# Kernel optimization log

Hardware: AMD Instinct MI355X
Metric: run time of the kernel (lower is better)

Reference implementation:

```python
import jax, jax.numpy as jnp
import numpy as np

G = 144          # fine grid size per axis
N = 200000       # active fine voxels
C_IN = 96
C_UP = C_IN // 3 # 32
C_OUT = 64
EPS = 1e-5


def _build_maps():
    rng = np.random.default_rng(0)
    lin = rng.choice(G ** 3, size=N, replace=False)
    coords = np.stack(np.unravel_index(lin, (G, G, G)), axis=1).astype(np.int64)  # [N,3]
    # coarse coords = unique parents (stride-2 downsample), inverse gives parent index per fine voxel
    coarse, up_src = np.unique(coords // 2, axis=0, return_inverse=True)
    up_off = ((coords[:, 0] % 2) * 2 + coords[:, 1] % 2) * 2 + coords[:, 2] % 2  # octant -> kernel offset id
    B = G + 2

    def enc(c):
        cc = c + 1
        return (cc[:, 0] * B + cc[:, 1]) * B + cc[:, 2]

    fkeys = enc(coords)
    order = np.argsort(fkeys)
    skeys = fkeys[order]
    offs = [(dx, dy, dz) for dx in (-1, 0, 1) for dy in (-1, 0, 1) for dz in (-1, 0, 1)]
    nbr = np.full((N, 27), -1, dtype=np.int32)
    for k, off in enumerate(offs):
        nk = enc(coords + np.asarray(off))
        pos = np.minimum(np.searchsorted(skeys, nk), N - 1)
        valid = skeys[pos] == nk
        nbr[:, k] = np.where(valid, order[pos].astype(np.int32), -1)
    return coarse.shape[0], up_src.astype(np.int32), up_off.astype(np.int32), nbr


def setup_inputs() -> dict:
    key = jax.random.key(0)
    ks = jax.random.split(key, 8)
    n_coarse, up_src, up_off, nbr = _build_maps()
    s_up = 1.0 / np.sqrt(8 * C_IN)
    s1 = 1.0 / np.sqrt(27 * C_IN)
    s2 = 1.0 / np.sqrt(27 * C_OUT)
    return {
        "x1_feats": jax.random.normal(ks[0], (n_coarse, C_IN), jnp.float32),
        "x2_feats": jax.random.normal(ks[1], (N, C_UP), jnp.float32),
        "x3_feats": jax.random.normal(ks[2], (N, C_UP), jnp.float32),
        "W_up": jax.random.normal(ks[3], (8, C_IN, C_UP), jnp.float32) * s_up,
        "g_up": jnp.ones((C_UP,), jnp.float32),
        "b_up": jnp.zeros((C_UP,), jnp.float32),
        "W1": jax.random.normal(ks[4], (27, C_IN, C_OUT), jnp.float32) * s1,
        "g1": jnp.ones((C_OUT,), jnp.float32),
        "b1": jnp.zeros((C_OUT,), jnp.float32),
        "W2": jax.random.normal(ks[5], (27, C_OUT, C_OUT), jnp.float32) * s2,
        "g2": jnp.ones((C_OUT,), jnp.float32),
        "b2": jnp.zeros((C_OUT,), jnp.float32),
        "up_src_idx": jnp.asarray(up_src),
        "up_off_id": jnp.asarray(up_off),
        "nbr_idx": jnp.asarray(nbr),
    }


def _bn_relu(x, g, b):
    # training-mode BatchNorm over active sites (biased var), then ReLU
    m = x.mean(0)
    v = x.var(0)
    return jax.nn.relu((x - m) * jax.lax.rsqrt(v + EPS) * g + b)


def _subm_conv(feats, W, nbr_idx):
    # 3x3x3 submanifold sparse conv: same coord set in/out; offset 13 is the center
    out = feats @ W[13]
    for k in range(27):
        if k == 13:
            continue
        idx = nbr_idx[:, k]
        valid = (idx >= 0)[:, None]
        g = jnp.where(valid, feats[jnp.maximum(idx, 0)], 0.0)
        out = out + g @ W[k]
    return out


def reference(x1_feats, x2_feats, x3_feats, W_up, g_up, b_up, W1, g1, b1, W2, g2, b2, up_src_idx, up_off_id, nbr_idx):
    # transposed conv k=2 s=2 (non-generative): each fine site reads its unique coarse parent,
    # weight selected by the octant offset id
    src = x1_feats[up_src_idx]  # [N, C_IN]
    up = jnp.zeros((src.shape[0], W_up.shape[2]), src.dtype)
    for k in range(8):
        up = up + jnp.where((up_off_id == k)[:, None], src @ W_up[k], 0.0)
    up = _bn_relu(up, g_up, b_up)
    x = jnp.concatenate([up, x2_feats, x3_feats], axis=1)  # [N, C_IN]
    x = _bn_relu(_subm_conv(x, W1, nbr_idx), g1, b1)
    x = _bn_relu(_subm_conv(x, W2, nbr_idx), g2, b2)
    return x
```

## Files before the change

kernel.cpp:

```cpp
#include <hip/hip_runtime.h>

typedef __attribute__((ext_vector_type(8))) short short8;
typedef __attribute__((ext_vector_type(4))) float floatx4;

__device__ inline unsigned short f2bf(float f) {
  union { float f; unsigned u; } x; x.f = f;
  unsigned r = x.u + 0x7FFFu + ((x.u >> 16) & 1u);
  return (unsigned short)(r >> 16);
}
__device__ inline float bf2f(unsigned short h) {
  union { unsigned u; float f; } x; x.u = ((unsigned)h) << 16;
  return x.f;
}

__global__ __launch_bounds__(256) void convw_kernel(const float* __restrict__ W1,
                                                    const float* __restrict__ W2,
                                                    const float* __restrict__ Wup,
                                                    unsigned short* __restrict__ W1t,
                                                    unsigned short* __restrict__ W2t,
                                                    unsigned short* __restrict__ Wupt,
                                                    float* __restrict__ parts) {
  int idx = blockIdx.x * 256 + threadIdx.x;
  const int n1 = 27 * 96 * 64;
  const int n2 = 27 * 64 * 64;
  const int n3 = 8 * 32 * 96;
  if (idx < n1) {
    int k = idx / (96 * 64);
    int r = idx % (96 * 64);
    int q = r / 64, c = r % 64;
    W1t[((size_t)k * 64 + c) * 96 + q] = f2bf(W1[idx]);
  } else if (idx < n1 + n2) {
    int j = idx - n1;
    int k = j / 4096;
    int r = j % 4096;
    int q = r / 64, c = r % 64;
    W2t[((size_t)k * 64 + c) * 64 + q] = f2bf(W2[j]);
  } else if (idx < n1 + n2 + n3) {
    int o = idx - n1 - n2;
    int k = o / 3072;
    int r = o % 3072;
    int c = r / 96, q = r % 96;
    Wupt[o] = f2bf(Wup[((size_t)k * 96 + q) * 32 + c]);
  } else if (idx < n1 + n2 + n3 + 320) {
    parts[idx - n1 - n2 - n3] = 0.f;
  }
}

__global__ __launch_bounds__(256) void up_mfma_kernel(const float* __restrict__ x1,
                                                      const int* __restrict__ up_src,
                                                      const int* __restrict__ up_off,
                                                      const unsigned short* __restrict__ Wupt,
                                                      float* __restrict__ up_raw,
                                                      float* __restrict__ part1,
                                                      float* __restrict__ part2,
                                                      int N) {
  constexpr int PAD = 104;
  __shared__ unsigned short Wl[8 * 32 * PAD];
  __shared__ float wsum[4][32];
  __shared__ float wsq[4][32];

  const int tid = threadIdx.x;
  const int wv = tid >> 6;
  const int lane = tid & 63;
  const int lr = lane & 15;
  const int lg = lane >> 4;

  for (int ch = tid; ch < 8 * 32 * 12; ch += 256) {
    int kc = ch / 12, j = ch % 12;
    short8 v = *(const short8*)(Wupt + (size_t)kc * 96 + j * 8);
    *(short8*)(&Wl[kc * PAD + j * 8]) = v;
  }
  __syncthreads();

  const int nTiles = (N + 63) >> 6;
  const short8 z8 = {0, 0, 0, 0, 0, 0, 0, 0};
  float cs[2] = {0.f, 0.f}, cq[2] = {0.f, 0.f};

  for (int tile = blockIdx.x; tile < nTiles; tile += gridDim.x) {
    const int base = tile * 64;
    const int r = base + wv * 16 + lr;
    int o = -100;
    const float* ptr = x1;
    if (r < N) {
      o = up_off[r];
      ptr = x1 + (size_t)up_src[r] * 96;
    }
    short8 a_all[3];
    #pragma unroll
    for (int s = 0; s < 3; ++s) {
      float4 f0 = *(const float4*)(ptr + s * 32 + lg * 8);
      float4 f1 = *(const float4*)(ptr + s * 32 + lg * 8 + 4);
      unsigned short u[8];
      u[0] = f2bf(f0.x); u[1] = f2bf(f0.y); u[2] = f2bf(f0.z); u[3] = f2bf(f0.w);
      u[4] = f2bf(f1.x); u[5] = f2bf(f1.y); u[6] = f2bf(f1.z); u[7] = f2bf(f1.w);
      a_all[s] = *(short8*)u;
    }
    if (r >= N) {
      #pragma unroll
      for (int s = 0; s < 3; ++s) a_all[s] = z8;
    }

    floatx4 acc[2];
    acc[0] = (floatx4){0.f, 0.f, 0.f, 0.f};
    acc[1] = (floatx4){0.f, 0.f, 0.f, 0.f};
    #pragma unroll
    for (int k = 0; k < 8; ++k) {
      bool sel = (o == k);
      #pragma unroll
      for (int s = 0; s < 3; ++s) {
        short8 af = sel ? a_all[s] : z8;
        #pragma unroll
        for (int ct = 0; ct < 2; ++ct) {
          short8 bf = *(const short8*)(&Wl[(k * 32 + ct * 16 + lr) * PAD + s * 32 + lg * 8]);
          acc[ct] = __builtin_amdgcn_mfma_f32_16x16x32_bf16(af, bf, acc[ct], 0, 0, 0);
        }
      }
    }
    #pragma unroll
    for (int ct = 0; ct < 2; ++ct) {
      #pragma unroll
      for (int reg = 0; reg < 4; ++reg) {
        float v = acc[ct][reg];
        int r2 = base + wv * 16 + lg * 4 + reg;
        if (r2 < N) up_raw[(size_t)r2 * 32 + ct * 16 + lr] = v;
        cs[ct] += v;
        cq[ct] += v * v;
      }
    }
  }

  #pragma unroll
  for (int ct = 0; ct < 2; ++ct) {
    float a = cs[ct], b = cq[ct];
    a += __shfl_xor(a, 16);
    a += __shfl_xor(a, 32);
    b += __shfl_xor(b, 16);
    b += __shfl_xor(b, 32);
    if (lg == 0) {
      wsum[wv][ct * 16 + lr] = a;
      wsq[wv][ct * 16 + lr] = b;
    }
  }
  __syncthreads();
  if (tid < 32) {
    float s1 = wsum[0][tid] + wsum[1][tid] + wsum[2][tid] + wsum[3][tid];
    float s2 = wsq[0][tid] + wsq[1][tid] + wsq[2][tid] + wsq[3][tid];
    atomicAdd(&part1[tid], s1);
    atomicAdd(&part2[tid], s2);
  }
}

__global__ __launch_bounds__(256) void concat_kernel(const float* __restrict__ up_raw,
                                                     const float* __restrict__ x2,
                                                     const float* __restrict__ x3,
                                                     const float* __restrict__ part1,
                                                     const float* __restrict__ part2,
                                                     const float* __restrict__ g,
                                                     const float* __restrict__ b,
                                                     unsigned short* __restrict__ xb,
                                                     int N) {
  __shared__ float ssb[64];
  if (threadIdx.x < 32) {
    int c = threadIdx.x;
    float mean = part1[c] / (float)N;
    float var = part2[c] / (float)N - mean * mean;
    float sc = g[c] * rsqrtf(var + 1e-5f);
    ssb[c] = sc;
    ssb[32 + c] = b[c] - mean * sc;
  }
  __syncthreads();
  int total = N * 12;
  for (int idx = blockIdx.x * 256 + threadIdx.x; idx < total; idx += gridDim.x * 256) {
    int row = idx / 12, p = idx % 12;
    float v[8];
    if (p < 4) {
      const float* s = up_raw + (size_t)row * 32 + p * 8;
      int c0 = p * 8;
      #pragma unroll
      for (int j = 0; j < 8; ++j) v[j] = fmaxf(s[j] * ssb[c0 + j] + ssb[32 + c0 + j], 0.f);
    } else if (p < 8) {
      const float* s = x2 + (size_t)row * 32 + (p - 4) * 8;
      #pragma unroll
      for (int j = 0; j < 8; ++j) v[j] = s[j];
    } else {
      const float* s = x3 + (size_t)row * 32 + (p - 8) * 8;
      #pragma unroll
      for (int j = 0; j < 8; ++j) v[j] = s[j];
    }
    unsigned short o[8];
    #pragma unroll
    for (int j = 0; j < 8; ++j) o[j] = f2bf(v[j]);
    ((uint4*)xb)[idx] = *(uint4*)o;
  }
}

template <int CIN, bool OUTBF>
__global__ __launch_bounds__(256) void conv_kernel(const unsigned short* __restrict__ feats,
                                                   const unsigned short* __restrict__ Wt,
                                                   const int* __restrict__ nbr,
                                                   void* __restrict__ yout,
                                                   float* __restrict__ part1,
                                                   float* __restrict__ part2,
                                                   int N) {
  constexpr int KS = CIN / 32;
  const int tid = threadIdx.x;
  const int wv = tid >> 6;
  const int lane = tid & 63;
  const int lr = lane & 15;
  const int lg = lane >> 4;
  const int wr = wv & 1;
  const int wc = wv >> 1;
  const int base = blockIdx.x * 128;
  const int rbase = base + wr * 64 + lr;
  const short8 z8 = {0, 0, 0, 0, 0, 0, 0, 0};

  floatx4 acc[4][2];
  #pragma unroll
  for (int m = 0; m < 4; ++m)
    #pragma unroll
    for (int ct = 0; ct < 2; ++ct) acc[m][ct] = (floatx4){0.f, 0.f, 0.f, 0.f};

  int nbc[4];
  #pragma unroll
  for (int m = 0; m < 4; ++m) {
    int r = rbase + m * 16;
    nbc[m] = (r < N) ? nbr[(size_t)r * 27] : -1;
  }

  #pragma unroll 1
  for (int t = 0; t < 27; ++t) {
    int nbn[4];
    int tn = (t < 26) ? t + 1 : 26;
    #pragma unroll
    for (int m = 0; m < 4; ++m) {
      int r = rbase + m * 16;
      nbn[m] = (r < N) ? nbr[(size_t)r * 27 + tn] : -1;
    }
    short8 A[4][KS];
    #pragma unroll
    for (int m = 0; m < 4; ++m) {
      #pragma unroll
      for (int s = 0; s < KS; ++s) A[m][s] = z8;
      if (nbc[m] >= 0) {
        const unsigned short* src = feats + (size_t)nbc[m] * CIN + lg * 8;
        #pragma unroll
        for (int s = 0; s < KS; ++s) A[m][s] = *(const short8*)(src + s * 32);
      }
    }
    bool any0 = __any(nbc[0] >= 0), any1 = __any(nbc[1] >= 0);
    bool any2 = __any(nbc[2] >= 0), any3 = __any(nbc[3] >= 0);
    if (any0 | any1 | any2 | any3) {
      short8 B[2][KS];
      const unsigned short* wsrc = Wt + ((size_t)t * 64 + wc * 32 + lr) * CIN + lg * 8;
      #pragma unroll
      for (int ct = 0; ct < 2; ++ct)
        #pragma unroll
        for (int s = 0; s < KS; ++s)
          B[ct][s] = *(const short8*)(wsrc + ct * 16 * CIN + s * 32);
      #pragma unroll
      for (int m = 0; m < 4; ++m) {
        bool anym = (m == 0) ? any0 : (m == 1) ? any1 : (m == 2) ? any2 : any3;
        if (anym) {
          #pragma unroll
          for (int s = 0; s < KS; ++s) {
            acc[m][0] = __builtin_amdgcn_mfma_f32_16x16x32_bf16(A[m][s], B[0][s], acc[m][0], 0, 0, 0);
            acc[m][1] = __builtin_amdgcn_mfma_f32_16x16x32_bf16(A[m][s], B[1][s], acc[m][1], 0, 0, 0);
          }
        }
      }
    }
    #pragma unroll
    for (int m = 0; m < 4; ++m) nbc[m] = nbn[m];
  }

  float cs[2] = {0.f, 0.f}, cq[2] = {0.f, 0.f};
  #pragma unroll
  for (int m = 0; m < 4; ++m) {
    #pragma unroll
    for (int ct = 0; ct < 2; ++ct) {
      #pragma unroll
      for (int reg = 0; reg < 4; ++reg) {
        float v = acc[m][ct][reg];
        int r = base + wr * 64 + m * 16 + lg * 4 + reg;
        int col = wc * 32 + ct * 16 + lr;
        if (r < N) {
          if (OUTBF)
            ((unsigned short*)yout)[(size_t)r * 64 + col] = f2bf(v);
          else
            ((float*)yout)[(size_t)r * 64 + col] = v;
        }
        cs[ct] += v;
        cq[ct] += v * v;
      }
    }
  }
  #pragma unroll
  for (int ct = 0; ct < 2; ++ct) {
    float a = cs[ct], b = cq[ct];
    a += __shfl_xor(a, 16);
    a += __shfl_xor(a, 32);
    b += __shfl_xor(b, 16);
    b += __shfl_xor(b, 32);
    if (lane < 16) {
      atomicAdd(&part1[wc * 32 + ct * 16 + lr], a);
      atomicAdd(&part2[wc * 32 + ct * 16 + lr], b);
    }
  }
}

__global__ __launch_bounds__(256) void apply_bn_bf16_inplace(unsigned short* __restrict__ y,
                                                             const float* __restrict__ part1,
                                                             const float* __restrict__ part2,
                                                             const float* __restrict__ g,
                                                             const float* __restrict__ b,
                                                             int N) {
  __shared__ float ssb[128];
  if (threadIdx.x < 64) {
    int c = threadIdx.x;
    float mean = part1[c] / (float)N;
    float var = part2[c] / (float)N - mean * mean;
    float sc = g[c] * rsqrtf(var + 1e-5f);
    ssb[c] = sc;
    ssb[64 + c] = b[c] - mean * sc;
  }
  __syncthreads();
  int total = N * 8;
  for (int idx = blockIdx.x * 256 + threadIdx.x; idx < total; idx += gridDim.x * 256) {
    int c0 = (idx & 7) * 8;
    uint4 d = ((uint4*)y)[idx];
    unsigned short* u = (unsigned short*)&d;
    #pragma unroll
    for (int j = 0; j < 8; ++j) {
      float f = bf2f(u[j]);
      f = fmaxf(f * ssb[c0 + j] + ssb[64 + c0 + j], 0.f);
      u[j] = f2bf(f);
    }
    ((uint4*)y)[idx] = d;
  }
}

__global__ __launch_bounds__(256) void apply_bn_inplace(float* __restrict__ y,
                                                        const float* __restrict__ part1,
                                                        const float* __restrict__ part2,
                                                        const float* __restrict__ g,
                                                        const float* __restrict__ b,
                                                        int N) {
  __shared__ float ssb[128];
  if (threadIdx.x < 64) {
    int c = threadIdx.x;
    float mean = part1[c] / (float)N;
    float var = part2[c] / (float)N - mean * mean;
    float sc = g[c] * rsqrtf(var + 1e-5f);
    ssb[c] = sc;
    ssb[64 + c] = b[c] - mean * sc;
  }
  __syncthreads();
  int total = N * 16;
  for (int idx = blockIdx.x * 256 + threadIdx.x; idx < total; idx += gridDim.x * 256) {
    int c0 = (idx & 15) * 4;
    float4 d = ((float4*)y)[idx];
    d.x = fmaxf(d.x * ssb[c0 + 0] + ssb[64 + c0 + 0], 0.f);
    d.y = fmaxf(d.y * ssb[c0 + 1] + ssb[64 + c0 + 1], 0.f);
    d.z = fmaxf(d.z * ssb[c0 + 2] + ssb[64 + c0 + 2], 0.f);
    d.w = fmaxf(d.w * ssb[c0 + 3] + ssb[64 + c0 + 3], 0.f);
    ((float4*)y)[idx] = d;
  }
}

extern "C" void kernel_launch(void* const* d_in, const int* in_sizes, int n_in,
                              void* d_out, int out_size, void* d_ws, size_t ws_size,
                              hipStream_t stream) {
  const float* x1 = (const float*)d_in[0];
  const float* x2 = (const float*)d_in[1];
  const float* x3 = (const float*)d_in[2];
  const float* Wup = (const float*)d_in[3];
  const float* gup = (const float*)d_in[4];
  const float* bup = (const float*)d_in[5];
  const float* W1 = (const float*)d_in[6];
  const float* g1 = (const float*)d_in[7];
  const float* b1 = (const float*)d_in[8];
  const float* W2 = (const float*)d_in[9];
  const float* g2 = (const float*)d_in[10];
  const float* b2 = (const float*)d_in[11];
  const int* up_src = (const int*)d_in[12];
  const int* up_off = (const int*)d_in[13];
  const int* nbr = (const int*)d_in[14];

  const int N = in_sizes[12];
  const int NB2 = (N + 127) / 128;

  char* ws = (char*)d_ws;
  size_t off = 0;
  auto alloc = [&](size_t bytes) -> void* {
    void* p = ws + off;
    off = (off + bytes + 255) & ~(size_t)255;
    return p;
  };

  unsigned short* xb   = (unsigned short*)alloc((size_t)N * 96 * 2);
  unsigned short* y1b  = (unsigned short*)alloc((size_t)N * 64 * 2);
  float* up_raw        = (float*)alloc((size_t)N * 32 * 4);
  unsigned short* W1t  = (unsigned short*)alloc((size_t)27 * 64 * 96 * 2);
  unsigned short* W2t  = (unsigned short*)alloc((size_t)27 * 64 * 64 * 2);
  unsigned short* Wupt = (unsigned short*)alloc((size_t)8 * 32 * 96 * 2);
  float* parts         = (float*)alloc(320 * 4);
  (void)ws_size;

  float* upP1 = parts;
  float* upP2 = parts + 32;
  float* c1P1 = parts + 64;
  float* c1P2 = parts + 128;
  float* c2P1 = parts + 192;
  float* c2P2 = parts + 256;

  float* out = (float*)d_out;

  convw_kernel<<<1178, 256, 0, stream>>>(W1, W2, Wup, W1t, W2t, Wupt, parts);
  up_mfma_kernel<<<1024, 256, 0, stream>>>(x1, up_src, up_off, Wupt, up_raw, upP1, upP2, N);
  concat_kernel<<<2048, 256, 0, stream>>>(up_raw, x2, x3, upP1, upP2, gup, bup, xb, N);
  conv_kernel<96, true><<<NB2, 256, 0, stream>>>(xb, W1t, nbr, y1b, c1P1, c1P2, N);
  apply_bn_bf16_inplace<<<2048, 256, 0, stream>>>(y1b, c1P1, c1P2, g1, b1, N);
  conv_kernel<64, false><<<NB2, 256, 0, stream>>>(y1b, W2t, nbr, out, c2P1, c2P2, N);
  apply_bn_inplace<<<2048, 256, 0, stream>>>(out, c2P1, c2P2, g2, b2, N);
}
```

Measured before the change: 598.3 us.

## Retile sparse conv to 16 rows per wave with double-buffered gather

The conv kernel now gives each wave 16 output rows and all 64 output columns, using 64-row blocks instead of 128, so each wave holds 4 accumulators rather than 8. The neighbor feature gather for offset t+1 is double-buffered and issued before the MFMAs for offset t, and neighbor indices are prefetched two steps ahead. This is meant to hide gather latency and raise occupancy via launch_bounds(256,4). In exchange, each wave now loads all 64 weight columns per offset, so weight traffic per row doubles, and the per-wave skip check covers only 16 rows.

```diff
diff --git a/kernel.cpp b/kernel.cpp
--- a/kernel.cpp
+++ b/kernel.cpp
@@ -195,115 +195,104 @@
 }
 
 template <int CIN, bool OUTBF>
-__global__ __launch_bounds__(256) void conv_kernel(const unsigned short* __restrict__ feats,
-                                                   const unsigned short* __restrict__ Wt,
-                                                   const int* __restrict__ nbr,
-                                                   void* __restrict__ yout,
-                                                   float* __restrict__ part1,
-                                                   float* __restrict__ part2,
-                                                   int N) {
+__global__ __launch_bounds__(256, 4) void conv_kernel(const unsigned short* __restrict__ feats,
+                                                      const unsigned short* __restrict__ Wt,
+                                                      const int* __restrict__ nbr,
+                                                      void* __restrict__ yout,
+                                                      float* __restrict__ part1,
+                                                      float* __restrict__ part2,
+                                                      int N) {
   constexpr int KS = CIN / 32;
   const int tid = threadIdx.x;
   const int wv = tid >> 6;
   const int lane = tid & 63;
   const int lr = lane & 15;
   const int lg = lane >> 4;
-  const int wr = wv & 1;
-  const int wc = wv >> 1;
-  const int base = blockIdx.x * 128;
-  const int rbase = base + wr * 64 + lr;
+  const int base = blockIdx.x * 64;
+  const int r = base + wv * 16 + lr;
+  const bool inb = (r < N);
+  const int* nrow = nbr + (size_t)r * 27;
   const short8 z8 = {0, 0, 0, 0, 0, 0, 0, 0};
 
-  floatx4 acc[4][2];
+  floatx4 acc[4];
   #pragma unroll
-  for (int m = 0; m < 4; ++m)
-    #pragma unroll
-    for (int ct = 0; ct < 2; ++ct) acc[m][ct] = (floatx4){0.f, 0.f, 0.f, 0.f};
-
-  int nbc[4];
+  for (int ct = 0; ct < 4; ++ct) acc[ct] = (floatx4){0.f, 0.f, 0.f, 0.f};
+
+  short8 Aa[KS], Ab[KS];
+  int idx_cur, idx_next;
+
+  idx_cur = inb ? nrow[0] : -1;
   #pragma unroll
-  for (int m = 0; m < 4; ++m) {
-    int r = rbase + m * 16;
-    nbc[m] = (r < N) ? nbr[(size_t)r * 27] : -1;
-  }
-
-  #pragma unroll 1
-  for (int t = 0; t < 27; ++t) {
-    int nbn[4];
-    int tn = (t < 26) ? t + 1 : 26;
-    #pragma unroll
-    for (int m = 0; m < 4; ++m) {
-      int r = rbase + m * 16;
-      nbn[m] = (r < N) ? nbr[(size_t)r * 27 + tn] : -1;
-    }
-    short8 A[4][KS];
-    #pragma unroll
-    for (int m = 0; m < 4; ++m) {
-      #pragma unroll
-      for (int s = 0; s < KS; ++s) A[m][s] = z8;
-      if (nbc[m] >= 0) {
-        const unsigned short* src = feats + (size_t)nbc[m] * CIN + lg * 8;
-        #pragma unroll
-        for (int s = 0; s < KS; ++s) A[m][s] = *(const short8*)(src + s * 32);
-      }
-    }
-    bool any0 = __any(nbc[0] >= 0), any1 = __any(nbc[1] >= 0);
-    bool any2 = __any(nbc[2] >= 0), any3 = __any(nbc[3] >= 0);
-    if (any0 | any1 | any2 | any3) {
-      short8 B[2][KS];
-      const unsigned short* wsrc = Wt + ((size_t)t * 64 + wc * 32 + lr) * CIN + lg * 8;
-      #pragma unroll
-      for (int ct = 0; ct < 2; ++ct)
+  for (int s = 0; s < KS; ++s) Aa[s] = z8;
+  if (idx_cur >= 0) {
+    const unsigned short* src = feats + (size_t)idx_cur * CIN + lg * 8;
+    #pragma unroll
+    for (int s = 0; s < KS; ++s) Aa[s] = *(const short8*)(src + s * 32);
+  }
+  idx_next = inb ? nrow[1] : -1;
+
+  auto STEP = [&](int t, short8 (&Ac)[KS], short8 (&An)[KS]) {
+    int idx_n2 = (inb && t + 2 < 27) ? nrow[t + 2] : -1;
+    #pragma unroll
+    for (int s = 0; s < KS; ++s) An[s] = z8;
+    if (idx_next >= 0) {
+      const unsigned short* src = feats + (size_t)idx_next * CIN + lg * 8;
+      #pragma unroll
+      for (int s = 0; s < KS; ++s) An[s] = *(const short8*)(src + s * 32);
+    }
+    if (__any(idx_cur >= 0)) {
+      short8 B[4][KS];
+      const unsigned short* wsrc = Wt + ((size_t)t * 64 + lr) * CIN + lg * 8;
+      #pragma unroll
+      for (int ct = 0; ct < 4; ++ct)
         #pragma unroll
         for (int s = 0; s < KS; ++s)
           B[ct][s] = *(const short8*)(wsrc + ct * 16 * CIN + s * 32);
       #pragma unroll
-      for (int m = 0; m < 4; ++m) {
-        bool anym = (m == 0) ? any0 : (m == 1) ? any1 : (m == 2) ? any2 : any3;
-        if (anym) {
-          #pragma unroll
-          for (int s = 0; s < KS; ++s) {
-            acc[m][0] = __builtin_amdgcn_mfma_f32_16x16x32_bf16(A[m][s], B[0][s], acc[m][0], 0, 0, 0);
-            acc[m][1] = __builtin_amdgcn_mfma_f32_16x16x32_bf16(A[m][s], B[1][s], acc[m][1], 0, 0, 0);
-          }
-        }
+      for (int s = 0; s < KS; ++s)
+        #pragma unroll
+        for (int ct = 0; ct < 4; ++ct)
+          acc[ct] = __builtin_amdgcn_mfma_f32_16x16x32_bf16(Ac[s], B[ct][s], acc[ct], 0, 0, 0);
+    }
+    idx_cur = idx_next;
+    idx_next = idx_n2;
+  };
+
+  #pragma unroll 1
+  for (int t = 0; t < 26; t += 2) {
+    STEP(t, Aa, Ab);
+    STEP(t + 1, Ab, Aa);
+  }
+  STEP(26, Aa, Ab);
+
+  float cs[4] = {0.f, 0.f, 0.f, 0.f}, cq[4] = {0.f, 0.f, 0.f, 0.f};
+  #pragma unroll
+  for (int ct = 0; ct < 4; ++ct) {
+    #pragma unroll
+    for (int reg = 0; reg < 4; ++reg) {
+      float v = acc[ct][reg];
+      int r2 = base + wv * 16 + lg * 4 + reg;
+      int col = ct * 16 + lr;
+      if (r2 < N) {
+        if (OUTBF)
+          ((unsigned short*)yout)[(size_t)r2 * 64 + col] = f2bf(v);
+        else
+          ((float*)yout)[(size_t)r2 * 64 + col] = v;
       }
-    }
-    #pragma unroll
-    for (int m = 0; m < 4; ++m) nbc[m] = nbn[m];
-  }
-
-  float cs[2] = {0.f, 0.f}, cq[2] = {0.f, 0.f};
+      cs[ct] += v;
+      cq[ct] += v * v;
+    }
+  }
   #pragma unroll
-  for (int m = 0; m < 4; ++m) {
-    #pragma unroll
-    for (int ct = 0; ct < 2; ++ct) {
-      #pragma unroll
-      for (int reg = 0; reg < 4; ++reg) {
-        float v = acc[m][ct][reg];
-        int r = base + wr * 64 + m * 16 + lg * 4 + reg;
-        int col = wc * 32 + ct * 16 + lr;
-        if (r < N) {
-          if (OUTBF)
-            ((unsigned short*)yout)[(size_t)r * 64 + col] = f2bf(v);
-          else
-            ((float*)yout)[(size_t)r * 64 + col] = v;
-        }
-        cs[ct] += v;
-        cq[ct] += v * v;
-      }
-    }
-  }
-  #pragma unroll
-  for (int ct = 0; ct < 2; ++ct) {
+  for (int ct = 0; ct < 4; ++ct) {
     float a = cs[ct], b = cq[ct];
     a += __shfl_xor(a, 16);
     a += __shfl_xor(a, 32);
     b += __shfl_xor(b, 16);
     b += __shfl_xor(b, 32);
     if (lane < 16) {
-      atomicAdd(&part1[wc * 32 + ct * 16 + lr], a);
-      atomicAdd(&part2[wc * 32 + ct * 16 + lr], b);
+      atomicAdd(&part1[ct * 16 + lr], a);
+      atomicAdd(&part2[ct * 16 + lr], b);
     }
   }
 }
@@ -387,7 +376,7 @@
   const int* nbr = (const int*)d_in[14];
 
   const int N = in_sizes[12];
-  const int NB2 = (N + 127) / 128;
+  const int NB = (N + 63) / 64;
 
   char* ws = (char*)d_ws;
   size_t off = 0;
@@ -418,8 +407,8 @@
   convw_kernel<<<1178, 256, 0, stream>>>(W1, W2, Wup, W1t, W2t, Wupt, parts);
   up_mfma_kernel<<<1024, 256, 0, stream>>>(x1, up_src, up_off, Wupt, up_raw, upP1, upP2, N);
   concat_kernel<<<2048, 256, 0, stream>>>(up_raw, x2, x3, upP1, upP2, gup, bup, xb, N);
-  conv_kernel<96, true><<<NB2, 256, 0, stream>>>(xb, W1t, nbr, y1b, c1P1, c1P2, N);
+  conv_kernel<96, true><<<NB, 256, 0, stream>>>(xb, W1t, nbr, y1b, c1P1, c1P2, N);
   apply_bn_bf16_inplace<<<2048, 256, 0, stream>>>(y1b, c1P1, c1P2, g1, b1, N);
-  conv_kernel<64, false><<<NB2, 256, 0, stream>>>(y1b, W2t, nbr, out, c2P1, c2P2, N);
+  conv_kernel<64, false><<<NB, 256, 0, stream>>>(y1b, W2t, nbr, out, c2P1, c2P2, N);
   apply_bn_inplace<<<2048, 256, 0, stream>>>(out, c2P1, c2P2, g2, b2, N);
 }
```

Result: slower. 1.003 ms (+67.6%).
